# Kernel tuning notes

Hardware: AMD Instinct MI355X
Metric: run time of the kernel (lower is better)

## Reference

```python
import jax, jax.numpy as jnp
import numpy as np

H = 1024        # hidden_size
NH = 16         # num_attention_heads
HD = H // NH    # attention_head_size = 64
EPS = 1e-12


def setup_inputs() -> dict:
    key = jax.random.key(0)
    ks = jax.random.split(key, 12)
    B, S = 2, 2048
    s = 0.02
    return {
        "hidden_states": jax.random.normal(ks[0], (B, S, H), jnp.float32),
        "attention_mask": jnp.zeros((B, 1, 1, S), jnp.float32),
        "Wq": jax.random.normal(ks[1], (H, H), jnp.float32) * s,
        "bq": jnp.zeros((H,), jnp.float32),
        "Wk": jax.random.normal(ks[2], (H, H), jnp.float32) * s,
        "bk": jnp.zeros((H,), jnp.float32),
        "Wv": jax.random.normal(ks[3], (H, H), jnp.float32) * s,
        "bv": jnp.zeros((H,), jnp.float32),
        "Wd": jax.random.normal(ks[4], (H, H), jnp.float32) * s,
        "bd": jnp.zeros((H,), jnp.float32),
        "ln_gamma": jnp.ones((H,), jnp.float32),
        "ln_beta": jnp.zeros((H,), jnp.float32),
    }


def _split_heads(x):
    # [B,S,H] -> [B,NH,S,HD]
    B, S, _ = x.shape
    return x.reshape(B, S, NH, HD).transpose(0, 2, 1, 3)


def reference(hidden_states, attention_mask, Wq, bq, Wk, bk, Wv, bv, Wd, bd, ln_gamma, ln_beta):
    q = _split_heads(hidden_states @ Wq.T + bq)
    k = _split_heads(hidden_states @ Wk.T + bk)
    v = _split_heads(hidden_states @ Wv.T + bv)

    scores = jnp.einsum("bhqd,bhkd->bhqk", q, k) / jnp.sqrt(jnp.float32(HD))
    scores = scores + attention_mask
    probs = jax.nn.softmax(scores, axis=-1)  # attention dropout p=0

    ctx = jnp.einsum("bhqk,bhkd->bhqd", probs, v)
    B, _, S, _ = ctx.shape
    ctx = ctx.transpose(0, 2, 1, 3).reshape(B, S, H)

    proj = ctx @ Wd.T + bd  # output dropout p=0
    x = hidden_states + proj
    mu = jnp.mean(x, axis=-1, keepdims=True)
    var = jnp.mean(jnp.square(x - mu), axis=-1, keepdims=True)
    out = (x - mu) * jax.lax.rsqrt(var + EPS) * ln_gamma + ln_beta
    return out
```

## Files before the change

### kernel.cpp

```cpp
#include <hip/hip_runtime.h>

typedef unsigned short u16;
typedef unsigned int u32;
typedef __attribute__((ext_vector_type(4))) unsigned short u16x4;
typedef __attribute__((ext_vector_type(8))) unsigned short u16x8;
typedef __attribute__((ext_vector_type(8))) __bf16 bf16x8;
typedef __attribute__((ext_vector_type(4))) float f32x4;
typedef __attribute__((ext_vector_type(16))) float f32x16;
typedef __attribute__((ext_vector_type(2))) int i32x2;

#define S_LEN 2048
#define HDIM 1024
#define NHEAD 16
#define HD 64
#define MTOK 4096
#define QKV_STRIDE 4194304
#define LOG2E 1.44269504089f
#define QKSCL (0.125f * 1.44269504089f)

__device__ __forceinline__ float bf2f(u16 h) {
    unsigned u = ((unsigned)h) << 16;
    return __builtin_bit_cast(float, u);
}
__device__ __forceinline__ u16 f2bf(float f) {
    return __builtin_bit_cast(u16, (__bf16)f);
}
__device__ __forceinline__ bf16x8 as_bf16(u16x8 u) {
    union { u16x8 a; bf16x8 b; } c; c.a = u; return c.b;
}
__device__ __forceinline__ void gld_lds16(const u16* g, u16* l) {
    __builtin_amdgcn_global_load_lds((const __attribute__((address_space(1))) u16*)g,
                                     (__attribute__((address_space(3))) u16*)l, 16, 0, 0);
}

__device__ __forceinline__ void pl32swap(u32& a, u32& b) {
#if __has_builtin(__builtin_amdgcn_permlane32_swap)
    i32x2 r = __builtin_amdgcn_permlane32_swap((int)a, (int)b, false, false);
    a = (u32)r[0]; b = (u32)r[1];
#else
    u32 as = (u32)__shfl_xor((int)a, 32);
    u32 bs = (u32)__shfl_xor((int)b, 32);
    bool hi = (threadIdx.x & 32) != 0;
    u32 na = hi ? bs : a;
    u32 nb = hi ? b : as;
    a = na; b = nb;
#endif
}

__device__ __forceinline__ void cast4(const float* __restrict__ s, u16* __restrict__ d, int i) {
    f32x4 v = *(const f32x4*)(s + (size_t)i * 4);
    u16x4 o;
    o[0] = f2bf(v[0]); o[1] = f2bf(v[1]); o[2] = f2bf(v[2]); o[3] = f2bf(v[3]);
    *(u16x4*)(d + (size_t)i * 4) = o;
}

__global__ __launch_bounds__(256) void prep(const float* __restrict__ hs,
                                            const float* __restrict__ Wq, const float* __restrict__ Wk,
                                            const float* __restrict__ Wv, const float* __restrict__ Wd,
                                            const float* __restrict__ bq, const float* __restrict__ bk,
                                            const float* __restrict__ bv,
                                            u16* __restrict__ hsb, u16* __restrict__ wqkvb,
                                            u16* __restrict__ wdb, float* __restrict__ b3) {
    int bid = blockIdx.x, tid = threadIdx.x;
    if (bid < 4096) {
        cast4(hs, hsb, bid * 256 + tid);
    } else if (bid < 5120) {
        cast4(Wq, wqkvb, (bid - 4096) * 256 + tid);
    } else if (bid < 6144) {
        cast4(Wk, wqkvb + HDIM * HDIM, (bid - 5120) * 256 + tid);
    } else if (bid < 7168) {
        cast4(Wv, wqkvb + 2 * HDIM * HDIM, (bid - 6144) * 256 + tid);
    } else if (bid < 8192) {
        cast4(Wd, wdb, (bid - 7168) * 256 + tid);
    } else {
        int i = (bid - 8192) * 256 + tid;
        if (i < 3072) b3[i] = (i < 1024) ? bq[i] : (i < 2048) ? bk[i - 1024] : bv[i - 2048];
    }
}

template <int MODE>
__global__ __launch_bounds__(256, 3) void gemm_bt(const u16* __restrict__ A, const u16* __restrict__ Bw,
                                                  const float* __restrict__ bias,
                                                  u16* __restrict__ outb, u16* __restrict__ vtout,
                                                  float* __restrict__ outf,
                                                  int Md, int Nd, int Kd) {
    __shared__ alignas(16) u16 As[2][128 * 32];
    __shared__ alignas(16) u16 Bs[2][128 * 32];
    const int tid = threadIdx.x;
    const int wave = tid >> 6, lane = tid & 63;
    const int l15 = lane & 15, l4 = lane >> 4;
    const int m0 = blockIdx.y * 128, n0 = blockIdx.x * 128;
    const int wm = wave >> 1, wn = wave & 1;

    const int cc0 = wave * 2;
    const int srow = lane >> 2;
    const int sco = (lane & 3) * 8;

    f32x4 acc[4][4];
#pragma unroll
    for (int i = 0; i < 4; i++)
#pragma unroll
        for (int j = 0; j < 4; j++) acc[i][j] = (f32x4){0.f, 0.f, 0.f, 0.f};

    auto STAGE = [&](int k0, int buf) {
#pragma unroll
        for (int i = 0; i < 2; i++) {
            int cc = cc0 + i;
            int row = cc * 16 + srow;
            gld_lds16(A + (size_t)(m0 + row) * Kd + k0 + sco, &As[buf][cc * 512]);
            gld_lds16(Bw + (size_t)(n0 + row) * Kd + k0 + sco, &Bs[buf][cc * 512]);
        }
    };

    const int nt = Kd >> 5;
    STAGE(0, 0);
    for (int t = 0; t < nt; ++t) {
        __builtin_amdgcn_s_barrier();
        if (t + 1 < nt) {
            STAGE((t + 1) << 5, (t + 1) & 1);
            asm volatile("s_waitcnt vmcnt(4)" ::: "memory");
        } else {
            asm volatile("s_waitcnt vmcnt(0)" ::: "memory");
        }
        __builtin_amdgcn_s_barrier();
        const u16* as = &As[t & 1][0];
        const u16* bs = &Bs[t & 1][0];
        bf16x8 af[4], bf[4];
#pragma unroll
        for (int x = 0; x < 4; x++) {
            af[x] = as_bf16(*(const u16x8*)&as[(wm * 64 + x * 16 + l15) * 32 + l4 * 8]);
            bf[x] = as_bf16(*(const u16x8*)&bs[(wn * 64 + x * 16 + l15) * 32 + l4 * 8]);
        }
        __builtin_amdgcn_s_setprio(1);
#pragma unroll
        for (int mi = 0; mi < 4; mi++)
#pragma unroll
            for (int nj = 0; nj < 4; nj++)
                acc[mi][nj] = __builtin_amdgcn_mfma_f32_16x16x32_bf16(af[mi], bf[nj], acc[mi][nj], 0, 0, 0);
        __builtin_amdgcn_s_setprio(0);
    }

#pragma unroll
    for (int mi = 0; mi < 4; mi++) {
#pragma unroll
        for (int nj = 0; nj < 4; nj++) {
            int coln = n0 + wn * 64 + nj * 16 + l15;
            float bv_ = bias[coln];
            int rowb = m0 + wm * 64 + mi * 16 + l4 * 4;
            if (MODE == 0) {
                int which = coln >> 10, nn = coln & 1023;
                int hh = nn >> 6, dd = nn & 63;
                int bb = rowb >> 11, ss = rowb & 2047;
                if (which < 2) {
#pragma unroll
                    for (int r = 0; r < 4; r++)
                        outb[(size_t)which * QKV_STRIDE + ((size_t)((bb << 4) + hh) * S_LEN + ss + r) * HD + dd] =
                            f2bf(acc[mi][nj][r] + bv_);
                } else {
                    u16x4 o;
#pragma unroll
                    for (int r = 0; r < 4; r++) o[r] = f2bf(acc[mi][nj][r] + bv_);
                    *(u16x4*)(vtout + ((size_t)((bb << 4) + hh) * HD + dd) * S_LEN + ss) = o;
                }
            } else {
#pragma unroll
                for (int r = 0; r < 4; r++)
                    outf[(size_t)(rowb + r) * Nd + coln] = acc[mi][nj][r] + bv_;
            }
        }
    }
}

__global__ __launch_bounds__(512, 4) void flash_attn6(const u16* __restrict__ qkv,
                                                      const u16* __restrict__ vt,
                                                      const float* __restrict__ amask,
                                                      u16* __restrict__ ctx) {
    __shared__ alignas(16) char smem[73728];

    const int tid = threadIdx.x;
    const int wave = tid >> 6, lane = tid & 63;
    const int l31 = lane & 31;
    const int hi = lane >> 5;
    const int hi4 = hi * 4;
    const int ws = wave & 3;
    const int g = wave >> 2;

    const int lid = blockIdx.x;
    const int idx = lid >> 3;
    const int bh = (lid & 7) * 4 + (idx >> 4);
    const int qx = idx & 15;
    const int b = bh >> 4, h = bh & 15;
    const int qr0 = qx * 128 + ws * 32;

    const u16* qh = qkv + (size_t)bh * (S_LEN * HD);
    const u16* kh = qh + QKV_STRIDE;
    const u16* vth = vt + (size_t)bh * (S_LEN * HD);

    u16* kbase = (u16*)(smem + g * 32768);
    u16* vbase = kbase + 8192;
    float* Ml = (float*)(smem + 65536);

    {
        f32x4 m = *(const f32x4*)(amask + (size_t)b * S_LEN + tid * 4);
#pragma unroll
        for (int j = 0; j < 4; j++) m[j] *= LOG2E;
        *(f32x4*)&Ml[tid * 4] = m;
    }

    bf16x8 qf[4];
#pragma unroll
    for (int s = 0; s < 4; ++s)
        qf[s] = as_bf16(*(const u16x8*)(qh + (size_t)(qr0 + l31) * HD + s * 16 + hi * 8));

    __syncthreads();

    const int srow = lane >> 3;
    const int schunk = (lane & 7) ^ srow;
    const u16* kss = kh + (size_t)(ws * 16 + srow) * HD + schunk * 8;
    const u16* vss = vth + (size_t)(ws * 16 + srow) * S_LEN + schunk * 8;

    f32x16 oacc[2];
#pragma unroll
    for (int d = 0; d < 2; ++d)
#pragma unroll
        for (int i = 0; i < 16; ++i) oacc[d][i] = 0.f;
    float l_run = 0.f;

    auto STAGE = [&](int tloc, int buf) {
        const int kv0 = ((tloc << 1) + g) << 6;
        const u16* ks = kss + (size_t)kv0 * HD;
        const u16* vs = vss + kv0;
        u16* kd = kbase + buf * 4096 + ws * 1024;
        u16* vd = vbase + buf * 4096 + ws * 1024;
        gld_lds16(ks, kd);
        gld_lds16(ks + 8 * HD, kd + 512);
        gld_lds16(vs, vd);
        gld_lds16(vs + 8 * S_LEN, vd + 512);
    };

    auto tile = [&](int tloc, int buf) {
        const int kv0 = ((tloc << 1) + g) << 6;
        const u16* kb = kbase + buf * 4096;
        const u16* vb = vbase + buf * 4096;
#pragma unroll
        for (int sub = 0; sub < 2; ++sub) {
            f32x16 accs;
#pragma unroll
            for (int i = 0; i < 16; ++i) accs[i] = 0.f;
            const int kvrow = sub * 32 + l31;
            const int ksw = (kvrow & 7) << 3;
            __builtin_amdgcn_s_setprio(1);
#pragma unroll
            for (int s = 0; s < 4; ++s) {
                bf16x8 kf = as_bf16(*(const u16x8*)&kb[kvrow * 64 + (((s * 2 + hi) << 3) ^ ksw)]);
                accs = __builtin_amdgcn_mfma_f32_32x32x16_bf16(kf, qf[s], accs, 0, 0, 0);
            }
            __builtin_amdgcn_s_setprio(0);
            u32 pw_[8];
#pragma unroll
            for (int rg = 0; rg < 4; ++rg) {
                f32x4 mk = *(const f32x4*)&Ml[kv0 + sub * 32 + rg * 8 + hi4];
#pragma unroll
                for (int r2 = 0; r2 < 2; ++r2) {
                    float pa = __builtin_amdgcn_exp2f(accs[rg * 4 + r2 * 2] * QKSCL + mk[r2 * 2]);
                    float pb = __builtin_amdgcn_exp2f(accs[rg * 4 + r2 * 2 + 1] * QKSCL + mk[r2 * 2 + 1]);
                    l_run += pa + pb;
                    pw_[rg * 2 + r2] = (u32)f2bf(pa) | ((u32)f2bf(pb) << 16);
                }
            }
            pl32swap(pw_[0], pw_[2]);
            pl32swap(pw_[1], pw_[3]);
            pl32swap(pw_[4], pw_[6]);
            pl32swap(pw_[5], pw_[7]);
            union { u32 w[4]; u16x8 v; } f0, f1;
            f0.w[0] = pw_[0]; f0.w[1] = pw_[1]; f0.w[2] = pw_[2]; f0.w[3] = pw_[3];
            f1.w[0] = pw_[4]; f1.w[1] = pw_[5]; f1.w[2] = pw_[6]; f1.w[3] = pw_[7];
            bf16x8 pf0 = as_bf16(f0.v), pf1 = as_bf16(f1.v);
            __builtin_amdgcn_s_setprio(1);
#pragma unroll
            for (int dsub = 0; dsub < 2; ++dsub) {
                const int drow = dsub * 32 + l31;
                const int dsw = (drow & 7) << 3;
                const int c0 = (sub * 4 + hi) << 3;
                const int c1 = ((sub * 2 + 1) * 2 + hi) << 3;
                bf16x8 vf0 = as_bf16(*(const u16x8*)&vb[drow * 64 + (c0 ^ dsw)]);
                oacc[dsub] = __builtin_amdgcn_mfma_f32_32x32x16_bf16(vf0, pf0, oacc[dsub], 0, 0, 0);
                bf16x8 vf1 = as_bf16(*(const u16x8*)&vb[drow * 64 + (c1 ^ dsw)]);
                oacc[dsub] = __builtin_amdgcn_mfma_f32_32x32x16_bf16(vf1, pf1, oacc[dsub], 0, 0, 0);
            }
            __builtin_amdgcn_s_setprio(0);
        }
    };

    STAGE(0, 0);
    for (int t = 0; t < 16; ++t) {
        __builtin_amdgcn_s_barrier();
        if (t + 1 < 16) {
            STAGE(t + 1, (t + 1) & 1);
            asm volatile("s_waitcnt vmcnt(4)" ::: "memory");
        } else {
            asm volatile("s_waitcnt vmcnt(0)" ::: "memory");
        }
        __builtin_amdgcn_s_barrier();
        tile(t, t & 1);
    }

    float* Oex = (float*)smem;
    float* lsum = (float*)(smem + 32768);
    __syncthreads();
    if (g == 1) {
#pragma unroll
        for (int dsub = 0; dsub < 2; ++dsub)
#pragma unroll
            for (int rg = 0; rg < 4; ++rg)
#pragma unroll
                for (int rr = 0; rr < 4; ++rr) {
                    int d = dsub * 32 + hi4 + rr + 8 * rg;
                    Oex[ws * 2048 + d * 32 + l31] = oacc[dsub][rg * 4 + rr];
                }
        float lB = l_run + __shfl_xor(l_run, 32);
        if (lane < 32) lsum[ws * 32 + lane] = lB;
    }
    __syncthreads();
    if (g == 0) {
        float lt = l_run + __shfl_xor(l_run, 32) + lsum[ws * 32 + l31];
        float inv = 1.0f / lt;
        u16* cp = ctx + ((size_t)b * S_LEN + qr0 + l31) * HDIM + h * HD;
#pragma unroll
        for (int dsub = 0; dsub < 2; ++dsub)
#pragma unroll
            for (int rg = 0; rg < 4; ++rg) {
                u16x4 o;
#pragma unroll
                for (int rr = 0; rr < 4; ++rr) {
                    int d = dsub * 32 + hi4 + rr + 8 * rg;
                    float v = oacc[dsub][rg * 4 + rr] + Oex[ws * 2048 + d * 32 + l31];
                    o[rr] = f2bf(v * inv);
                }
                *(u16x4*)(cp + dsub * 32 + hi4 + 8 * rg) = o;
            }
    }
}

__global__ __launch_bounds__(256) void resid_ln(const float* __restrict__ hs, const float* __restrict__ proj,
                                                const float* __restrict__ g, const float* __restrict__ be,
                                                float* __restrict__ out) {
    int row = blockIdx.x, tid = threadIdx.x;
    int base = row * HDIM + tid * 4;
    f32x4 a = *(const f32x4*)(hs + base);
    f32x4 p = *(const f32x4*)(proj + base);
    f32x4 x = a + p;
    float s = x[0] + x[1] + x[2] + x[3];
    float sq = x[0] * x[0] + x[1] * x[1] + x[2] * x[2] + x[3] * x[3];
#pragma unroll
    for (int m = 1; m < 64; m <<= 1) {
        s += __shfl_xor(s, m);
        sq += __shfl_xor(sq, m);
    }
    __shared__ float red[8];
    int wave = tid >> 6, lane = tid & 63;
    if (lane == 0) { red[wave] = s; red[4 + wave] = sq; }
    __syncthreads();
    s = red[0] + red[1] + red[2] + red[3];
    sq = red[4] + red[5] + red[6] + red[7];
    float mean = s * (1.0f / 1024.0f);
    float var = sq * (1.0f / 1024.0f) - mean * mean;
    float rstd = rsqrtf(fmaxf(var, 0.f) + 1e-12f);
    f32x4 gg = *(const f32x4*)(g + tid * 4);
    f32x4 bb = *(const f32x4*)(be + tid * 4);
    f32x4 o;
#pragma unroll
    for (int j = 0; j < 4; j++) o[j] = (x[j] - mean) * rstd * gg[j] + bb[j];
    *(f32x4*)(out + base) = o;
}

extern "C" void kernel_launch(void* const* d_in, const int* in_sizes, int n_in,
                              void* d_out, int out_size, void* d_ws, size_t ws_size,
                              hipStream_t stream) {
    const float* hs    = (const float*)d_in[0];
    const float* amask = (const float*)d_in[1];
    const float* Wq    = (const float*)d_in[2];
    const float* bq    = (const float*)d_in[3];
    const float* Wk    = (const float*)d_in[4];
    const float* bk    = (const float*)d_in[5];
    const float* Wv    = (const float*)d_in[6];
    const float* bv    = (const float*)d_in[7];
    const float* Wd    = (const float*)d_in[8];
    const float* bd    = (const float*)d_in[9];
    const float* gamma = (const float*)d_in[10];
    const float* beta  = (const float*)d_in[11];

    char* ws = (char*)d_ws;
    u16*   hsb   = (u16*)(ws);
    u16*   Wqkvb = (u16*)(ws + ((size_t)8 << 20));
    u16*   Wdb   = (u16*)(ws + ((size_t)14 << 20));
    u16*   qkv   = (u16*)(ws + ((size_t)16 << 20));
    u16*   vt    = qkv + 2 * (size_t)QKV_STRIDE;
    u16*   ctx   = (u16*)(ws + ((size_t)40 << 20));
    float* proj  = (float*)(ws + ((size_t)48 << 20));
    float* b3    = (float*)(ws + ((size_t)64 << 20));

    prep<<<8204, 256, 0, stream>>>(hs, Wq, Wk, Wv, Wd, bq, bk, bv, hsb, Wqkvb, Wdb, b3);

    gemm_bt<0><<<dim3(24, 32), 256, 0, stream>>>(hsb, Wqkvb, b3, qkv, vt, nullptr, MTOK, 3072, HDIM);

    flash_attn6<<<512, 512, 0, stream>>>(qkv, vt, amask, ctx);

    gemm_bt<1><<<dim3(8, 32), 256, 0, stream>>>(ctx, Wdb, bd, nullptr, nullptr, proj, MTOK, HDIM, HDIM);

    resid_ln<<<MTOK, 256, 0, stream>>>(hs, proj, gamma, beta, (float*)d_out);
}
```

Baseline: 129.2 us.

## Drop intra-block KV split in flash attention; use 4-wave blocks over full KV

The attention kernel no longer splits the KV sequence between two wave groups that merge partial outputs through shared memory at the end. Each block now has 4 waves that walk all 32 KV tiles serially with double buffering, which removes the cross-group reduction, the extra barriers and about half the LDS per block. This allows more blocks per CU, but each wave's serial loop becomes twice as long and each block has fewer waves to hide latency. The scale-and-mask step is also rewritten as 2-wide float vector operations, presumably to encourage packed FMA/add instructions.

```diff
diff --git a/kernel.cpp b/kernel.cpp
--- a/kernel.cpp
+++ b/kernel.cpp
@@ -5,6 +5,7 @@
 typedef __attribute__((ext_vector_type(4))) unsigned short u16x4;
 typedef __attribute__((ext_vector_type(8))) unsigned short u16x8;
 typedef __attribute__((ext_vector_type(8))) __bf16 bf16x8;
+typedef __attribute__((ext_vector_type(2))) float f32x2;
 typedef __attribute__((ext_vector_type(4))) float f32x4;
 typedef __attribute__((ext_vector_type(16))) float f32x16;
 typedef __attribute__((ext_vector_type(2))) int i32x2;
@@ -171,19 +172,20 @@
     }
 }
 
-__global__ __launch_bounds__(512, 4) void flash_attn6(const u16* __restrict__ qkv,
+__global__ __launch_bounds__(256, 4) void flash_attn7(const u16* __restrict__ qkv,
                                                       const u16* __restrict__ vt,
                                                       const float* __restrict__ amask,
                                                       u16* __restrict__ ctx) {
-    __shared__ alignas(16) char smem[73728];
+    __shared__ alignas(16) u16 Kb[2][4096];
+    __shared__ alignas(16) u16 Vb[2][4096];
+    __shared__ float Ml[2048];
 
     const int tid = threadIdx.x;
     const int wave = tid >> 6, lane = tid & 63;
     const int l31 = lane & 31;
     const int hi = lane >> 5;
     const int hi4 = hi * 4;
-    const int ws = wave & 3;
-    const int g = wave >> 2;
+    const int ws = wave;
 
     const int lid = blockIdx.x;
     const int idx = lid >> 3;
@@ -196,15 +198,13 @@
     const u16* kh = qh + QKV_STRIDE;
     const u16* vth = vt + (size_t)bh * (S_LEN * HD);
 
-    u16* kbase = (u16*)(smem + g * 32768);
-    u16* vbase = kbase + 8192;
-    float* Ml = (float*)(smem + 65536);
-
     {
-        f32x4 m = *(const f32x4*)(amask + (size_t)b * S_LEN + tid * 4);
-#pragma unroll
-        for (int j = 0; j < 4; j++) m[j] *= LOG2E;
-        *(f32x4*)&Ml[tid * 4] = m;
+        f32x4 m0 = *(const f32x4*)(amask + (size_t)b * S_LEN + tid * 8);
+        f32x4 m1 = *(const f32x4*)(amask + (size_t)b * S_LEN + tid * 8 + 4);
+#pragma unroll
+        for (int j = 0; j < 4; j++) { m0[j] *= LOG2E; m1[j] *= LOG2E; }
+        *(f32x4*)&Ml[tid * 8] = m0;
+        *(f32x4*)&Ml[tid * 8 + 4] = m1;
     }
 
     bf16x8 qf[4];
@@ -224,24 +224,24 @@
     for (int d = 0; d < 2; ++d)
 #pragma unroll
         for (int i = 0; i < 16; ++i) oacc[d][i] = 0.f;
-    float l_run = 0.f;
-
-    auto STAGE = [&](int tloc, int buf) {
-        const int kv0 = ((tloc << 1) + g) << 6;
+    f32x2 l2 = (f32x2){0.f, 0.f};
+
+    auto STAGE = [&](int t, int buf) {
+        const int kv0 = t << 6;
         const u16* ks = kss + (size_t)kv0 * HD;
         const u16* vs = vss + kv0;
-        u16* kd = kbase + buf * 4096 + ws * 1024;
-        u16* vd = vbase + buf * 4096 + ws * 1024;
+        u16* kd = &Kb[buf][ws * 1024];
+        u16* vd = &Vb[buf][ws * 1024];
         gld_lds16(ks, kd);
         gld_lds16(ks + 8 * HD, kd + 512);
         gld_lds16(vs, vd);
         gld_lds16(vs + 8 * S_LEN, vd + 512);
     };
 
-    auto tile = [&](int tloc, int buf) {
-        const int kv0 = ((tloc << 1) + g) << 6;
-        const u16* kb = kbase + buf * 4096;
-        const u16* vb = vbase + buf * 4096;
+    auto tile = [&](int t, int buf) {
+        const int kv0 = t << 6;
+        const u16* kb = &Kb[buf][0];
+        const u16* vb = &Vb[buf][0];
 #pragma unroll
         for (int sub = 0; sub < 2; ++sub) {
             f32x16 accs;
@@ -262,9 +262,15 @@
                 f32x4 mk = *(const f32x4*)&Ml[kv0 + sub * 32 + rg * 8 + hi4];
 #pragma unroll
                 for (int r2 = 0; r2 < 2; ++r2) {
-                    float pa = __builtin_amdgcn_exp2f(accs[rg * 4 + r2 * 2] * QKSCL + mk[r2 * 2]);
-                    float pb = __builtin_amdgcn_exp2f(accs[rg * 4 + r2 * 2 + 1] * QKSCL + mk[r2 * 2 + 1]);
-                    l_run += pa + pb;
+                    f32x2 sa;
+                    sa[0] = accs[rg * 4 + r2 * 2];
+                    sa[1] = accs[rg * 4 + r2 * 2 + 1];
+                    f32x2 mm; mm[0] = mk[r2 * 2]; mm[1] = mk[r2 * 2 + 1];
+                    sa = sa * QKSCL + mm;
+                    float pa = __builtin_amdgcn_exp2f(sa[0]);
+                    float pb = __builtin_amdgcn_exp2f(sa[1]);
+                    f32x2 pp; pp[0] = pa; pp[1] = pb;
+                    l2 += pp;
                     pw_[rg * 2 + r2] = (u32)f2bf(pa) | ((u32)f2bf(pb) << 16);
                 }
             }
@@ -293,9 +299,9 @@
     };
 
     STAGE(0, 0);
-    for (int t = 0; t < 16; ++t) {
+    for (int t = 0; t < 32; ++t) {
         __builtin_amdgcn_s_barrier();
-        if (t + 1 < 16) {
+        if (t + 1 < 32) {
             STAGE(t + 1, (t + 1) & 1);
             asm volatile("s_waitcnt vmcnt(4)" ::: "memory");
         } else {
@@ -305,41 +311,20 @@
         tile(t, t & 1);
     }
 
-    float* Oex = (float*)smem;
-    float* lsum = (float*)(smem + 32768);
-    __syncthreads();
-    if (g == 1) {
-#pragma unroll
-        for (int dsub = 0; dsub < 2; ++dsub)
-#pragma unroll
-            for (int rg = 0; rg < 4; ++rg)
-#pragma unroll
-                for (int rr = 0; rr < 4; ++rr) {
-                    int d = dsub * 32 + hi4 + rr + 8 * rg;
-                    Oex[ws * 2048 + d * 32 + l31] = oacc[dsub][rg * 4 + rr];
-                }
-        float lB = l_run + __shfl_xor(l_run, 32);
-        if (lane < 32) lsum[ws * 32 + lane] = lB;
-    }
-    __syncthreads();
-    if (g == 0) {
-        float lt = l_run + __shfl_xor(l_run, 32) + lsum[ws * 32 + l31];
-        float inv = 1.0f / lt;
-        u16* cp = ctx + ((size_t)b * S_LEN + qr0 + l31) * HDIM + h * HD;
-#pragma unroll
-        for (int dsub = 0; dsub < 2; ++dsub)
-#pragma unroll
-            for (int rg = 0; rg < 4; ++rg) {
-                u16x4 o;
-#pragma unroll
-                for (int rr = 0; rr < 4; ++rr) {
-                    int d = dsub * 32 + hi4 + rr + 8 * rg;
-                    float v = oacc[dsub][rg * 4 + rr] + Oex[ws * 2048 + d * 32 + l31];
-                    o[rr] = f2bf(v * inv);
-                }
-                *(u16x4*)(cp + dsub * 32 + hi4 + 8 * rg) = o;
-            }
-    }
+    float l = l2[0] + l2[1];
+    l += __shfl_xor(l, 32);
+    float inv = 1.0f / l;
+    u16* cp = ctx + ((size_t)b * S_LEN + qr0 + l31) * HDIM + h * HD;
+#pragma unroll
+    for (int dsub = 0; dsub < 2; ++dsub)
+#pragma unroll
+        for (int rg = 0; rg < 4; ++rg) {
+            u16x4 o;
+#pragma unroll
+            for (int rr = 0; rr < 4; ++rr)
+                o[rr] = f2bf(oacc[dsub][rg * 4 + rr] * inv);
+            *(u16x4*)(cp + dsub * 32 + hi4 + 8 * rg) = o;
+        }
 }
 
 __global__ __launch_bounds__(256) void resid_ln(const float* __restrict__ hs, const float* __restrict__ proj,
@@ -404,7 +389,7 @@
 
     gemm_bt<0><<<dim3(24, 32), 256, 0, stream>>>(hsb, Wqkvb, b3, qkv, vt, nullptr, MTOK, 3072, HDIM);
 
-    flash_attn6<<<512, 512, 0, stream>>>(qkv, vt, amask, ctx);
+    flash_attn7<<<512, 256, 0, stream>>>(qkv, vt, amask, ctx);
 
     gemm_bt<1><<<dim3(8, 32), 256, 0, stream>>>(ctx, Wdb, bd, nullptr, nullptr, proj, MTOK, HDIM, HDIM);
 
```

Result: slower. 135.7 us (+5.0%).

## Use 256x256 pipelined QKV GEMM kernel and store projection output in bf16

Applied to the files above, without the earlier changes.

Replaces the generic 128x128 QKV GEMM with a dedicated 512-thread kernel that computes 256x256 output tiles. It uses 64-wide K stages, direct global-to-LDS loads, XOR-swizzled LDS, a deeper prefetch pipeline with explicit vmcnt waits, and block-index remapping for cache locality. The goal is more data reuse per tile and fewer wave stalls on memory, at the cost of more registers and only 192 blocks. The output projection now writes bf16 instead of fp32, which halves the traffic read by the residual LayerNorm but adds rounding error to the projection result.

```diff
diff --git a/kernel.cpp b/kernel.cpp
--- a/kernel.cpp
+++ b/kernel.cpp
@@ -5,6 +5,7 @@
 typedef __attribute__((ext_vector_type(4))) unsigned short u16x4;
 typedef __attribute__((ext_vector_type(8))) unsigned short u16x8;
 typedef __attribute__((ext_vector_type(8))) __bf16 bf16x8;
+typedef __attribute__((ext_vector_type(2))) float f32x2;
 typedef __attribute__((ext_vector_type(4))) float f32x4;
 typedef __attribute__((ext_vector_type(16))) float f32x16;
 typedef __attribute__((ext_vector_type(2))) int i32x2;
@@ -78,12 +79,129 @@
     }
 }
 
-template <int MODE>
-__global__ __launch_bounds__(256, 3) void gemm_bt(const u16* __restrict__ A, const u16* __restrict__ Bw,
-                                                  const float* __restrict__ bias,
-                                                  u16* __restrict__ outb, u16* __restrict__ vtout,
-                                                  float* __restrict__ outf,
-                                                  int Md, int Nd, int Kd) {
+__global__ __launch_bounds__(512, 2) void gemm_qkv8(const u16* __restrict__ A, const u16* __restrict__ Bw,
+                                                    const float* __restrict__ bias,
+                                                    u16* __restrict__ outb, u16* __restrict__ vtout) {
+    __shared__ alignas(16) u16 lds[65536];
+
+    const int tid = threadIdx.x, wave = tid >> 6, lane = tid & 63;
+    const int l15 = lane & 15, l4 = lane >> 4;
+    const int wm = wave >> 2, wn = wave & 3;
+
+    const int wid = (blockIdx.x & 7) * 24 + (blockIdx.x >> 3);
+    const int m0 = (wid / 12) * 256, n0 = (wid % 12) * 256;
+
+    f32x4 acc[8][4];
+#pragma unroll
+    for (int i = 0; i < 8; i++)
+#pragma unroll
+        for (int j = 0; j < 4; j++) acc[i][j] = (f32x4){0.f, 0.f, 0.f, 0.f};
+
+    const int srow_lo = wave * 8 + (lane >> 3);
+    const int scolL = (lane & 7) * 8;
+    auto STAGE = [&](int s) {
+        if (s > 63) return;
+        const int T = s >> 2, h = s & 3;
+        const u16* G = (h < 2) ? A : Bw;
+        const int grow0 = ((h < 2) ? m0 : n0) + (h & 1) * 128;
+        u16* reg = &lds[(T & 1) * 32768 + (h >> 1) * 16384 + (h & 1) * 8192];
+#pragma unroll
+        for (int j = 0; j < 2; j++) {
+            int row = j * 64 + srow_lo;
+            int cg = scolL ^ (((row >> 2) & 1) << 4);
+            gld_lds16(G + (size_t)(grow0 + row) * 1024 + T * 64 + cg, reg + j * 4096 + wave * 512);
+        }
+    };
+
+    bf16x8 afr[4], bfr[4];
+    auto PULLA = [&](int T, int mh, int ks) {
+        const u16* r = &lds[(T & 1) * 32768 + wm * 8192];
+#pragma unroll
+        for (int mi = 0; mi < 4; mi++) {
+            int rr = mh * 64 + mi * 16 + l15;
+            int col = (ks * 32 + l4 * 8) ^ (((rr >> 2) & 1) << 4);
+            afr[mi] = as_bf16(*(const u16x8*)&r[rr * 64 + col]);
+        }
+    };
+    auto PULLB = [&](int T, int ks) {
+        const u16* r = &lds[(T & 1) * 32768 + 16384 + (wn >> 1) * 8192];
+#pragma unroll
+        for (int nj = 0; nj < 4; nj++) {
+            int rr = (wn & 1) * 64 + nj * 16 + l15;
+            int col = (ks * 32 + l4 * 8) ^ (((rr >> 2) & 1) << 4);
+            bfr[nj] = as_bf16(*(const u16x8*)&r[rr * 64 + col]);
+        }
+    };
+    auto MFMA16 = [&](int mh) {
+        __builtin_amdgcn_s_setprio(1);
+#pragma unroll
+        for (int mi = 0; mi < 4; mi++)
+#pragma unroll
+            for (int nj = 0; nj < 4; nj++)
+                acc[mh * 4 + mi][nj] = __builtin_amdgcn_mfma_f32_16x16x32_bf16(afr[mi], bfr[nj], acc[mh * 4 + mi][nj], 0, 0, 0);
+        __builtin_amdgcn_s_setprio(0);
+    };
+
+    for (int s = 0; s < 7; ++s) STAGE(s);
+    asm volatile("s_waitcnt vmcnt(6)" ::: "memory");
+    __builtin_amdgcn_s_barrier();
+
+    for (int T = 0; T < 16; ++T) {
+        PULLA(T, 0, 0); PULLB(T, 0);
+        STAGE(4 * T + 7);
+        __builtin_amdgcn_s_barrier();
+        MFMA16(0);
+        __builtin_amdgcn_s_barrier();
+        PULLA(T, 1, 0);
+        STAGE(4 * T + 8);
+        __builtin_amdgcn_s_barrier();
+        MFMA16(1);
+        __builtin_amdgcn_s_barrier();
+        PULLA(T, 0, 1); PULLB(T, 1);
+        STAGE(4 * T + 9);
+        __builtin_amdgcn_s_barrier();
+        MFMA16(0);
+        __builtin_amdgcn_s_barrier();
+        PULLA(T, 1, 1);
+        STAGE(4 * T + 10);
+        if (T < 14) {
+            asm volatile("s_waitcnt vmcnt(6)" ::: "memory");
+        } else {
+            asm volatile("s_waitcnt vmcnt(0)" ::: "memory");
+        }
+        __builtin_amdgcn_s_barrier();
+        MFMA16(1);
+        __builtin_amdgcn_s_barrier();
+    }
+
+#pragma unroll
+    for (int mi = 0; mi < 8; mi++) {
+#pragma unroll
+        for (int nj = 0; nj < 4; nj++) {
+            int coln = n0 + wn * 64 + nj * 16 + l15;
+            float bv_ = bias[coln];
+            int rowb = m0 + wm * 128 + mi * 16 + l4 * 4;
+            int which = coln >> 10, nn = coln & 1023;
+            int hh = nn >> 6, dd = nn & 63;
+            int bb = rowb >> 11, ss = rowb & 2047;
+            if (which < 2) {
+#pragma unroll
+                for (int r = 0; r < 4; r++)
+                    outb[(size_t)which * QKV_STRIDE + ((size_t)((bb << 4) + hh) * S_LEN + ss + r) * HD + dd] =
+                        f2bf(acc[mi][nj][r] + bv_);
+            } else {
+                u16x4 o;
+#pragma unroll
+                for (int r = 0; r < 4; r++) o[r] = f2bf(acc[mi][nj][r] + bv_);
+                *(u16x4*)(vtout + ((size_t)((bb << 4) + hh) * HD + dd) * S_LEN + ss) = o;
+            }
+        }
+    }
+}
+
+__global__ __launch_bounds__(256, 3) void gemm_proj(const u16* __restrict__ A, const u16* __restrict__ Bw,
+                                                    const float* __restrict__ bias,
+                                                    u16* __restrict__ outb, int Nd, int Kd) {
     __shared__ alignas(16) u16 As[2][128 * 32];
     __shared__ alignas(16) u16 Bs[2][128 * 32];
     const int tid = threadIdx.x;
@@ -147,26 +265,9 @@
             int coln = n0 + wn * 64 + nj * 16 + l15;
             float bv_ = bias[coln];
             int rowb = m0 + wm * 64 + mi * 16 + l4 * 4;
-            if (MODE == 0) {
-                int which = coln >> 10, nn = coln & 1023;
-                int hh = nn >> 6, dd = nn & 63;
-                int bb = rowb >> 11, ss = rowb & 2047;
-                if (which < 2) {
-#pragma unroll
-                    for (int r = 0; r < 4; r++)
-                        outb[(size_t)which * QKV_STRIDE + ((size_t)((bb << 4) + hh) * S_LEN + ss + r) * HD + dd] =
-                            f2bf(acc[mi][nj][r] + bv_);
-                } else {
-                    u16x4 o;
-#pragma unroll
-                    for (int r = 0; r < 4; r++) o[r] = f2bf(acc[mi][nj][r] + bv_);
-                    *(u16x4*)(vtout + ((size_t)((bb << 4) + hh) * HD + dd) * S_LEN + ss) = o;
-                }
-            } else {
-#pragma unroll
-                for (int r = 0; r < 4; r++)
-                    outf[(size_t)(rowb + r) * Nd + coln] = acc[mi][nj][r] + bv_;
-            }
+#pragma unroll
+            for (int r = 0; r < 4; r++)
+                outb[(size_t)(rowb + r) * Nd + coln] = f2bf(acc[mi][nj][r] + bv_);
         }
     }
 }
@@ -342,14 +443,16 @@
     }
 }
 
-__global__ __launch_bounds__(256) void resid_ln(const float* __restrict__ hs, const float* __restrict__ proj,
+__global__ __launch_bounds__(256) void resid_ln(const float* __restrict__ hs, const u16* __restrict__ proj,
                                                 const float* __restrict__ g, const float* __restrict__ be,
                                                 float* __restrict__ out) {
     int row = blockIdx.x, tid = threadIdx.x;
     int base = row * HDIM + tid * 4;
     f32x4 a = *(const f32x4*)(hs + base);
-    f32x4 p = *(const f32x4*)(proj + base);
-    f32x4 x = a + p;
+    u16x4 pb = *(const u16x4*)(proj + base);
+    f32x4 x;
+#pragma unroll
+    for (int j = 0; j < 4; j++) x[j] = a[j] + bf2f(pb[j]);
     float s = x[0] + x[1] + x[2] + x[3];
     float sq = x[0] * x[0] + x[1] * x[1] + x[2] * x[2] + x[3] * x[3];
 #pragma unroll
@@ -397,16 +500,16 @@
     u16*   qkv   = (u16*)(ws + ((size_t)16 << 20));
     u16*   vt    = qkv + 2 * (size_t)QKV_STRIDE;
     u16*   ctx   = (u16*)(ws + ((size_t)40 << 20));
-    float* proj  = (float*)(ws + ((size_t)48 << 20));
+    u16*   projb = (u16*)(ws + ((size_t)48 << 20));
     float* b3    = (float*)(ws + ((size_t)64 << 20));
 
     prep<<<8204, 256, 0, stream>>>(hs, Wq, Wk, Wv, Wd, bq, bk, bv, hsb, Wqkvb, Wdb, b3);
 
-    gemm_bt<0><<<dim3(24, 32), 256, 0, stream>>>(hsb, Wqkvb, b3, qkv, vt, nullptr, MTOK, 3072, HDIM);
+    gemm_qkv8<<<192, 512, 0, stream>>>(hsb, Wqkvb, b3, qkv, vt);
 
     flash_attn6<<<512, 512, 0, stream>>>(qkv, vt, amask, ctx);
 
-    gemm_bt<1><<<dim3(8, 32), 256, 0, stream>>>(ctx, Wdb, bd, nullptr, nullptr, proj, MTOK, HDIM, HDIM);
-
-    resid_ln<<<MTOK, 256, 0, stream>>>(hs, proj, gamma, beta, (float*)d_out);
-}
+    gemm_proj<<<dim3(8, 32), 256, 0, stream>>>(ctx, Wdb, bd, projb, HDIM, HDIM);
+
+    resid_ln<<<MTOK, 256, 0, stream>>>(hs, projb, gamma, beta, (float*)d_out);
+}
```

Result: no change. 129.4 us (+0.1%).
